# Kernel optimization log

Hardware: AMD Instinct MI355X
Metric: run time of the kernel (lower is better)

The kernel has to match this reference:

```python
import jax, jax.numpy as jnp
import numpy as np

FRONT_FRAC = 0.30   # fraction of lowest-score indices masked (student) / kept (teacher row 0)
RAND_FRAC = 0.10    # fraction of random indices additionally masked for student
# NOTE: the original teacher-mask loop has a reset bug: only row 0 of each batch
# element gets the 'keep only front indices' mask; rows 1..R-1 end up all ones.
# We replicate that behavior faithfully.

def setup_inputs() -> dict:
    key = jax.random.key(0)
    score = jax.random.normal(key, (8, 2048, 4096), dtype=jnp.float32)
    return {"score": score}

def _masks(score):
    B, R, C = score.shape
    k_front = int(C * FRONT_FRAC)
    k_rand = int(C * RAND_FRAC)
    # ascending sort -> indices of the k_front lowest scores per row  [B,R,k_front]
    front = jnp.argsort(score, axis=-1)[..., :k_front]
    # random.sample(range(C), k_rand) per row -> random permutation prefix
    rkey = jax.random.key(42)
    rand_idx = jnp.argsort(jax.random.uniform(rkey, (B, R, C)), axis=-1)[..., :k_rand]
    bb = jnp.arange(B)[:, None, None]
    rr = jnp.arange(R)[None, :, None]
    # student mask: ones, zeroed at front|random indices
    student_mask = jnp.ones((B, R, C), score.dtype)
    student_mask = student_mask.at[bb, rr, front].set(0)
    student_mask = student_mask.at[bb, rr, rand_idx].set(0)
    # teacher mask: row 0 = indicator of front indices; rows 1.. = all ones (original bug)
    teacher_mask = jnp.ones((B, R, C), score.dtype)
    teacher_mask = teacher_mask.at[:, 0, :].set(0)
    bb0 = jnp.arange(B)[:, None]
    teacher_mask = teacher_mask.at[bb0, 0, front[:, 0, :]].set(1)
    return student_mask, teacher_mask

def reference(score):
    B, R, C = score.shape
    student_mask, teacher_mask = _masks(score)
    student = score * student_mask
    teacher = score * teacher_mask
    # original: cat over batch -> [B*R,C], reshape(B,-1,R), transpose(1,2)
    student = student.reshape(B, -1, R).swapaxes(1, 2)
    teacher = teacher.reshape(B, -1, R).swapaxes(1, 2)
    return student, teacher
```

## Files before the change

### kernel.cpp

```cpp
#include <hip/hip_runtime.h>
#include <stdint.h>

#define BB 8
#define RR 2048
#define CC 4096
#define KFRONT 1228
#define KRAND  409
#define NT 256
#define EPT 16
#define ROWS 32
#define PAD 129

__device__ __forceinline__ uint32_t rotl32(uint32_t x, uint32_t r) {
  return (x << r) | (x >> (32u - r));
}

__device__ __forceinline__ uint32_t threefry_bits(uint32_t i) {
  const uint32_t ks0 = 0u, ks1 = 42u;
  const uint32_t ks2 = 0x1BD11BDAu ^ ks0 ^ ks1;
  uint32_t x0 = ks0;
  uint32_t x1 = i + ks1;
#define R4(a, b, c, d)                         \
  x0 += x1; x1 = rotl32(x1, (a)); x1 ^= x0;    \
  x0 += x1; x1 = rotl32(x1, (b)); x1 ^= x0;    \
  x0 += x1; x1 = rotl32(x1, (c)); x1 ^= x0;    \
  x0 += x1; x1 = rotl32(x1, (d)); x1 ^= x0;
  R4(13u, 15u, 26u, 6u)  x0 += ks1; x1 += ks2 + 1u;
  R4(17u, 29u, 16u, 24u) x0 += ks2; x1 += ks0 + 2u;
  R4(13u, 15u, 26u, 6u)  x0 += ks0; x1 += ks1 + 3u;
  R4(17u, 29u, 16u, 24u) x0 += ks1; x1 += ks2 + 4u;
  R4(13u, 15u, 26u, 6u)  x0 += ks2; x1 += ks0 + 5u;
#undef R4
  return x0 ^ x1;
}

struct SelSh {
  uint32_t hist4[4 * 256];
  uint32_t cum[256];
  int sel_digit;
  int sel_below;
};

template <int NPASS>
__device__ uint64_t radix_select(const uint32_t (&keys)[EPT], int tid, int k,
                                 SelSh* sh) {
  uint64_t prefix = 0;
  int kk = k;
  const int wave = tid >> 6;
  for (int p = NPASS - 1; p >= 0; --p) {
    const int shift = 8 * p;
    ((uint4*)sh->hist4)[tid] = make_uint4(0, 0, 0, 0);
    __syncthreads();
#pragma unroll
    for (int j = 0; j < EPT; ++j) {
      uint64_t comp = ((uint64_t)keys[j] << 12) | (uint32_t)(j * NT + tid);
      if ((comp >> (shift + 8)) == prefix)
        atomicAdd(&sh->hist4[wave * 256 + ((uint32_t)(comp >> shift) & 255u)],
                  1u);
    }
    __syncthreads();
    if (tid < 64) {
      uint4 h0 = ((const uint4*)(sh->hist4 + 0))[tid];
      uint4 h1 = ((const uint4*)(sh->hist4 + 256))[tid];
      uint4 h2 = ((const uint4*)(sh->hist4 + 512))[tid];
      uint4 h3 = ((const uint4*)(sh->hist4 + 768))[tid];
      uint32_t s0 = h0.x + h1.x + h2.x + h3.x;
      uint32_t s1 = h0.y + h1.y + h2.y + h3.y;
      uint32_t s2 = h0.z + h1.z + h2.z + h3.z;
      uint32_t s3 = h0.w + h1.w + h2.w + h3.w;
      uint32_t sum = s0 + s1 + s2 + s3;
      uint32_t inc = sum;
      for (int off = 1; off < 64; off <<= 1) {
        uint32_t v = __shfl_up(inc, (unsigned)off);
        if (tid >= off) inc += v;
      }
      uint32_t base = inc - sum;
      ((uint4*)sh->cum)[tid] =
          make_uint4(base + s0, base + s0 + s1, base + s0 + s1 + s2, base + sum);
    }
    __syncthreads();
    int cum = (int)sh->cum[tid];
    int prev = tid ? (int)sh->cum[tid - 1] : 0;
    if (cum >= kk && prev < kk) { sh->sel_digit = tid; sh->sel_below = prev; }
    __syncthreads();
    prefix = (prefix << 8) | (uint32_t)sh->sel_digit;
    kk -= sh->sel_below;
    __syncthreads();
  }
  return prefix;
}

__global__ __launch_bounds__(NT) void fused_kernel(
    const float* __restrict__ score, float* __restrict__ outS,
    float* __restrict__ outT) {
  __shared__ SelSh sh;
  __shared__ uint32_t zbits[ROWS][PAD];
  __shared__ uint32_t fbits[ROWS][PAD];
  __shared__ float tin[ROWS][PAD];

  const int tid = threadIdx.x;
  const int stripe = blockIdx.x;
  const int b = blockIdx.y;
  const int u0 = stripe * 64;
  const int r0 = u0 >> 1;

  for (int rr = 0; rr < ROWS; ++rr) {
    const int rowid = b * RR + (r0 + rr);
    const float* srow = score + (size_t)rowid * CC;
    uint32_t keyS[EPT], keyR[EPT];
#pragma unroll
    for (int j = 0; j < EPT; ++j) {
      int c = j * NT + tid;
      uint32_t fb = __float_as_uint(srow[c]);
      keyS[j] = fb ^ ((uint32_t)((int32_t)fb >> 31) | 0x80000000u);
      keyR[j] = threefry_bits((uint32_t)rowid * (uint32_t)CC + (uint32_t)c) >> 9;
    }
    uint64_t pivF = radix_select<6>(keyS, tid, KFRONT, &sh);
    uint64_t pivR = radix_select<5>(keyR, tid, KRAND, &sh);
#pragma unroll
    for (int j = 0; j < EPT; ++j) {
      int c = j * NT + tid;
      uint64_t compS = ((uint64_t)keyS[j] << 12) | (uint32_t)c;
      uint64_t compR = ((uint64_t)keyR[j] << 12) | (uint32_t)c;
      int isF = (compS <= pivF) ? 1 : 0;
      int isZ = (isF || (compR <= pivR)) ? 1 : 0;
      uint64_t bZ = __ballot(isZ);
      uint64_t bF = __ballot(isF);
      if ((tid & 31) == 0) {
        uint32_t wz = (tid & 32) ? (uint32_t)(bZ >> 32) : (uint32_t)bZ;
        uint32_t wf = (tid & 32) ? (uint32_t)(bF >> 32) : (uint32_t)bF;
        zbits[rr][c >> 5] = wz;
        fbits[rr][c >> 5] = wf;
      }
    }
  }
  __syncthreads();

  const int u_local = tid & 63;
  const int rl = u_local >> 1;
  const int half = u_local & 1;
  const bool isrow0 = (r0 + rl) == 0;
  float* oS = outS + (size_t)b * RR * CC + (size_t)(u0 + u_local);
  float* oT = outT + (size_t)b * RR * CC + (size_t)(u0 + u_local);

  for (int vt = 0; vt < 32; ++vt) {
    const int v0 = vt * 64;
#pragma unroll
    for (int it = 0; it < 16; ++it) {
      int idx = it * NT + tid;
      int lrl = idx >> 7;
      int colsel = (idx >> 6) & 1;
      int lane = idx & 63;
      tin[lrl][colsel * 64 + lane] =
          score[(size_t)(b * RR + r0 + lrl) * CC + colsel * 2048 + v0 + lane];
    }
    __syncthreads();
    const int w0 = half * 64 + (v0 >> 5);
    const uint32_t z0 = zbits[rl][w0], z1 = zbits[rl][w0 + 1];
    const uint32_t f0 = fbits[rl][w0], f1 = fbits[rl][w0 + 1];
#pragma unroll
    for (int it = 0; it < 16; ++it) {
      int vl = it * 4 + (tid >> 6);
      float s = tin[rl][half * 64 + vl];
      uint32_t zw = (vl & 32) ? z1 : z0;
      uint32_t fw = (vl & 32) ? f1 : f0;
      int bit = vl & 31;
      float st = ((zw >> bit) & 1u) ? 0.0f : s;
      float te = isrow0 ? ((((fw >> bit) & 1u)) ? s : 0.0f) : s;
      size_t o = (size_t)(v0 + vl) * CC;
      oS[o] = st;
      oT[o] = te;
    }
    __syncthreads();
  }
}

extern "C" void kernel_launch(void* const* d_in, const int* in_sizes, int n_in,
                              void* d_out, int out_size, void* d_ws,
                              size_t ws_size, hipStream_t stream) {
  const float* score = (const float*)d_in[0];
  float* outS = (float*)d_out;
  float* outT = outS + (size_t)BB * RR * CC;
  dim3 grid(RR / ROWS, BB);
  hipLaunchKernelGGL(fused_kernel, grid, dim3(NT), 0, stream, score, outS,
                     outT);
}
```

Baseline: 1.289 ms.

## Move radix select to per-wavefront rows with early exit and smaller stripes

Each wavefront now owns whole rows (4 rows per wave, 16 rows per block) and runs its radix select with a per-wave LDS histogram and shuffle/ballot scans. This removes the block-wide __syncthreads barriers inside every select pass. The first pass counts 4-bit digits in packed register counters before doing atomics. Passes exit early once the kth element is unique or at an extreme, found by a min/max reduction. Each lane holds 64 keys in registers, which raises register pressure. The output transpose now covers 32 columns per block, so stores are less contiguous per row, and occupancy is hinted at 4 blocks per SM.

Measured after the change: 2.553 ms. 98.1% more time.

```diff
diff --git a/kernel.cpp b/kernel.cpp
--- a/kernel.cpp
+++ b/kernel.cpp
@@ -7,9 +7,8 @@
 #define KFRONT 1228
 #define KRAND  409
 #define NT 256
-#define EPT 16
-#define ROWS 32
-#define PAD 129
+#define ROWS 16
+#define RPW 4
 
 __device__ __forceinline__ uint32_t rotl32(uint32_t x, uint32_t r) {
   return (x << r) | (x >> (32u - r));
@@ -34,140 +33,195 @@
   return x0 ^ x1;
 }
 
-struct SelSh {
-  uint32_t hist4[4 * 256];
-  uint32_t cum[256];
-  int sel_digit;
-  int sel_below;
-};
-
-template <int NPASS>
-__device__ uint64_t radix_select(const uint32_t (&keys)[EPT], int tid, int k,
-                                 SelSh* sh) {
+template <int NPASS, int NB1>
+__device__ __forceinline__ uint64_t wave_select(const uint32_t (&key)[64],
+                                                int lane, int k,
+                                                uint32_t* hist) {
   uint64_t prefix = 0;
+  uint64_t result = 0;
   int kk = k;
-  const int wave = tid >> 6;
-  for (int p = NPASS - 1; p >= 0; --p) {
+
+  auto pick = [&](int shift) -> bool {
+    const uint4 h = *(const uint4*)(hist + 4 * lane);
+    int s0 = (int)h.x, s1 = s0 + (int)h.y, s2 = s1 + (int)h.z,
+        s3 = s2 + (int)h.w;
+    int inc = s3;
+#pragma unroll
+    for (int off = 1; off < 64; off <<= 1) {
+      int v = __shfl_up(inc, (unsigned)off);
+      if (lane >= off) inc += v;
+    }
+    const int base = inc - s3;
+    const uint64_t bal = __ballot(base + s3 >= kk);
+    const int L = __ffsll((unsigned long long)bal) - 1;
+    const int bL = __shfl(base, L);
+    const int a0 = __shfl(s0, L), a1 = __shfl(s1, L), a2 = __shfl(s2, L),
+              a3 = __shfl(s3, L);
+    int dsub, below, cnt;
+    if (kk <= bL + a0)      { dsub = 0; below = bL;      cnt = a0;      }
+    else if (kk <= bL + a1) { dsub = 1; below = bL + a0; cnt = a1 - a0; }
+    else if (kk <= bL + a2) { dsub = 2; below = bL + a1; cnt = a2 - a1; }
+    else                    { dsub = 3; below = bL + a2; cnt = a3 - a2; }
+    prefix = (prefix << 8) | (uint32_t)(4 * L + dsub);
+    kk -= below;
+    if (shift == 0) { result = prefix; return true; }
+    if (cnt == 1 || kk == 1 || kk == cnt) {
+      const bool usemin = (kk == 1 && cnt > 1);
+      uint64_t found = usemin ? ~0ull : 0ull;
+#pragma unroll
+      for (int j = 0; j < 64; ++j) {
+        const uint64_t comp =
+            ((uint64_t)key[j] << 12) | (uint32_t)(j * 64 + lane);
+        if ((comp >> shift) == prefix)
+          found = usemin ? (comp < found ? comp : found)
+                         : (comp > found ? comp : found);
+      }
+#pragma unroll
+      for (int off = 1; off < 64; off <<= 1) {
+        const uint64_t o = (uint64_t)__shfl_xor((unsigned long long)found, off);
+        found = usemin ? (o < found ? o : found) : (o > found ? o : found);
+      }
+      result = found;
+      return true;
+    }
+    return false;
+  };
+
+  {
+    *(uint4*)(hist + 4 * lane) = make_uint4(0, 0, 0, 0);
+    const int ksh = 8 * NPASS - 20;
+    uint64_t c0 = 0, c1 = 0;
+#pragma unroll
+    for (int j = 0; j < 64; ++j) {
+      const uint32_t d = key[j] >> ksh;
+      if constexpr (NB1 <= 8) {
+        c0 += 1ull << (8 * d);
+      } else {
+        if (d < 8) c0 += 1ull << (8 * d);
+        else       c1 += 1ull << (8 * (d - 8));
+      }
+    }
+#pragma unroll
+    for (int b = 0; b < NB1; ++b) {
+      const uint32_t cv =
+          (uint32_t)(((b < 8) ? c0 : c1) >> (8 * (b & 7))) & 0xffu;
+      if (cv) atomicAdd(&hist[b], cv);
+    }
+    if (pick(8 * (NPASS - 1))) return result;
+  }
+#pragma unroll 1
+  for (int p = NPASS - 2; p >= 0; --p) {
     const int shift = 8 * p;
-    ((uint4*)sh->hist4)[tid] = make_uint4(0, 0, 0, 0);
-    __syncthreads();
-#pragma unroll
-    for (int j = 0; j < EPT; ++j) {
-      uint64_t comp = ((uint64_t)keys[j] << 12) | (uint32_t)(j * NT + tid);
+    *(uint4*)(hist + 4 * lane) = make_uint4(0, 0, 0, 0);
+#pragma unroll
+    for (int j = 0; j < 64; ++j) {
+      const uint64_t comp =
+          ((uint64_t)key[j] << 12) | (uint32_t)(j * 64 + lane);
       if ((comp >> (shift + 8)) == prefix)
-        atomicAdd(&sh->hist4[wave * 256 + ((uint32_t)(comp >> shift) & 255u)],
-                  1u);
-    }
-    __syncthreads();
-    if (tid < 64) {
-      uint4 h0 = ((const uint4*)(sh->hist4 + 0))[tid];
-      uint4 h1 = ((const uint4*)(sh->hist4 + 256))[tid];
-      uint4 h2 = ((const uint4*)(sh->hist4 + 512))[tid];
-      uint4 h3 = ((const uint4*)(sh->hist4 + 768))[tid];
-      uint32_t s0 = h0.x + h1.x + h2.x + h3.x;
-      uint32_t s1 = h0.y + h1.y + h2.y + h3.y;
-      uint32_t s2 = h0.z + h1.z + h2.z + h3.z;
-      uint32_t s3 = h0.w + h1.w + h2.w + h3.w;
-      uint32_t sum = s0 + s1 + s2 + s3;
-      uint32_t inc = sum;
-      for (int off = 1; off < 64; off <<= 1) {
-        uint32_t v = __shfl_up(inc, (unsigned)off);
-        if (tid >= off) inc += v;
-      }
-      uint32_t base = inc - sum;
-      ((uint4*)sh->cum)[tid] =
-          make_uint4(base + s0, base + s0 + s1, base + s0 + s1 + s2, base + sum);
-    }
-    __syncthreads();
-    int cum = (int)sh->cum[tid];
-    int prev = tid ? (int)sh->cum[tid - 1] : 0;
-    if (cum >= kk && prev < kk) { sh->sel_digit = tid; sh->sel_below = prev; }
-    __syncthreads();
-    prefix = (prefix << 8) | (uint32_t)sh->sel_digit;
-    kk -= sh->sel_below;
-    __syncthreads();
-  }
-  return prefix;
-}
-
-__global__ __launch_bounds__(NT) void fused_kernel(
+        atomicAdd(&hist[(uint32_t)(comp >> shift) & 255u], 1u);
+    }
+    if (pick(shift)) return result;
+  }
+  return result;
+}
+
+__global__ __launch_bounds__(NT, 4) void fused_kernel(
     const float* __restrict__ score, float* __restrict__ outS,
     float* __restrict__ outT) {
-  __shared__ SelSh sh;
-  __shared__ uint32_t zbits[ROWS][PAD];
-  __shared__ uint32_t fbits[ROWS][PAD];
-  __shared__ float tin[ROWS][PAD];
+  __shared__ __align__(16) uint32_t sh_hist[4 * 256];
+  __shared__ uint32_t zbT[128][17];
+  __shared__ uint32_t fb0[128];
+  __shared__ float tin[ROWS][130];
 
   const int tid = threadIdx.x;
+  const int lane = tid & 63;
+  const int wv = tid >> 6;
   const int stripe = blockIdx.x;
   const int b = blockIdx.y;
-  const int u0 = stripe * 64;
-  const int r0 = u0 >> 1;
-
-  for (int rr = 0; rr < ROWS; ++rr) {
-    const int rowid = b * RR + (r0 + rr);
+  const int r0 = stripe * ROWS;
+  const int u0 = 2 * r0;
+
+  uint32_t* hist = sh_hist + wv * 256;
+
+#pragma unroll 1
+  for (int t = 0; t < RPW; ++t) {
+    const int rl = wv * RPW + t;
+    const int rowid = b * RR + (r0 + rl);
     const float* srow = score + (size_t)rowid * CC;
-    uint32_t keyS[EPT], keyR[EPT];
-#pragma unroll
-    for (int j = 0; j < EPT; ++j) {
-      int c = j * NT + tid;
-      uint32_t fb = __float_as_uint(srow[c]);
-      keyS[j] = fb ^ ((uint32_t)((int32_t)fb >> 31) | 0x80000000u);
-      keyR[j] = threefry_bits((uint32_t)rowid * (uint32_t)CC + (uint32_t)c) >> 9;
-    }
-    uint64_t pivF = radix_select<6>(keyS, tid, KFRONT, &sh);
-    uint64_t pivR = radix_select<5>(keyR, tid, KRAND, &sh);
-#pragma unroll
-    for (int j = 0; j < EPT; ++j) {
-      int c = j * NT + tid;
-      uint64_t compS = ((uint64_t)keyS[j] << 12) | (uint32_t)c;
-      uint64_t compR = ((uint64_t)keyR[j] << 12) | (uint32_t)c;
-      int isF = (compS <= pivF) ? 1 : 0;
-      int isZ = (isF || (compR <= pivR)) ? 1 : 0;
-      uint64_t bZ = __ballot(isZ);
-      uint64_t bF = __ballot(isF);
-      if ((tid & 31) == 0) {
-        uint32_t wz = (tid & 32) ? (uint32_t)(bZ >> 32) : (uint32_t)bZ;
-        uint32_t wf = (tid & 32) ? (uint32_t)(bF >> 32) : (uint32_t)bF;
-        zbits[rr][c >> 5] = wz;
-        fbits[rr][c >> 5] = wf;
-      }
+    uint32_t key[64];
+#pragma unroll
+    for (int j = 0; j < 64; ++j) {
+      const uint32_t fb = __float_as_uint(srow[j * 64 + lane]);
+      key[j] = fb ^ ((uint32_t)((int32_t)fb >> 31) | 0x80000000u);
+    }
+    const uint64_t pivF = wave_select<6, 16>(key, lane, KFRONT, hist);
+    uint64_t fm = 0;
+#pragma unroll
+    for (int j = 0; j < 64; ++j) {
+      const uint64_t comp =
+          ((uint64_t)key[j] << 12) | (uint32_t)(j * 64 + lane);
+      fm |= (uint64_t)(comp <= pivF) << j;
+    }
+    if (r0 + rl == 0) {
+#pragma unroll
+      for (int j = 0; j < 64; ++j) {
+        const uint64_t bf = __ballot((fm >> j) & 1ull);
+        if ((lane & 31) == 0)
+          fb0[2 * j + (lane >> 5)] =
+              (lane & 32) ? (uint32_t)(bf >> 32) : (uint32_t)bf;
+      }
+    }
+#pragma unroll
+    for (int j = 0; j < 64; ++j)
+      key[j] = threefry_bits((uint32_t)rowid * (uint32_t)CC +
+                             (uint32_t)(j * 64 + lane)) >> 9;
+    const uint64_t pivR = wave_select<5, 8>(key, lane, KRAND, hist);
+#pragma unroll
+    for (int j = 0; j < 64; ++j) {
+      const uint64_t comp =
+          ((uint64_t)key[j] << 12) | (uint32_t)(j * 64 + lane);
+      const int isZ = (int)((fm >> j) & 1ull) | (int)(comp <= pivR);
+      const uint64_t bz = __ballot(isZ);
+      if ((lane & 31) == 0)
+        zbT[2 * j + (lane >> 5)][rl] =
+            (lane & 32) ? (uint32_t)(bz >> 32) : (uint32_t)bz;
     }
   }
   __syncthreads();
 
-  const int u_local = tid & 63;
-  const int rl = u_local >> 1;
-  const int half = u_local & 1;
-  const bool isrow0 = (r0 + rl) == 0;
-  float* oS = outS + (size_t)b * RR * CC + (size_t)(u0 + u_local);
-  float* oT = outT + (size_t)b * RR * CC + (size_t)(u0 + u_local);
-
+  const int ul = tid & 31;
+  const int rl2 = ul >> 1;
+  const int half = ul & 1;
+  const bool isrow0 = (r0 + rl2) == 0;
+  float* oS = outS + (size_t)b * RR * CC + (size_t)(u0 + ul);
+  float* oT = outT + (size_t)b * RR * CC + (size_t)(u0 + ul);
+
+#pragma unroll 1
   for (int vt = 0; vt < 32; ++vt) {
     const int v0 = vt * 64;
 #pragma unroll
-    for (int it = 0; it < 16; ++it) {
-      int idx = it * NT + tid;
-      int lrl = idx >> 7;
-      int colsel = (idx >> 6) & 1;
-      int lane = idx & 63;
-      tin[lrl][colsel * 64 + lane] =
-          score[(size_t)(b * RR + r0 + lrl) * CC + colsel * 2048 + v0 + lane];
+    for (int it = 0; it < 8; ++it) {
+      const int idx = it * NT + tid;
+      const int lrl = idx >> 7;
+      const int colsel = (idx >> 6) & 1;
+      const int ll = idx & 63;
+      tin[lrl][colsel * 64 + ll] =
+          score[(size_t)(b * RR + r0 + lrl) * CC + colsel * 2048 + v0 + ll];
     }
     __syncthreads();
     const int w0 = half * 64 + (v0 >> 5);
-    const uint32_t z0 = zbits[rl][w0], z1 = zbits[rl][w0 + 1];
-    const uint32_t f0 = fbits[rl][w0], f1 = fbits[rl][w0 + 1];
-#pragma unroll
-    for (int it = 0; it < 16; ++it) {
-      int vl = it * 4 + (tid >> 6);
-      float s = tin[rl][half * 64 + vl];
-      uint32_t zw = (vl & 32) ? z1 : z0;
-      uint32_t fw = (vl & 32) ? f1 : f0;
-      int bit = vl & 31;
-      float st = ((zw >> bit) & 1u) ? 0.0f : s;
-      float te = isrow0 ? ((((fw >> bit) & 1u)) ? s : 0.0f) : s;
-      size_t o = (size_t)(v0 + vl) * CC;
+    const uint32_t z0 = zbT[w0][rl2], z1 = zbT[w0 + 1][rl2];
+    const uint32_t f0 = fb0[w0], f1 = fb0[w0 + 1];
+#pragma unroll
+    for (int it = 0; it < 8; ++it) {
+      const int vl = it * 8 + (tid >> 5);
+      const float s = tin[rl2][half * 64 + vl];
+      const uint32_t zw = (vl & 32) ? z1 : z0;
+      const uint32_t fw = (vl & 32) ? f1 : f0;
+      const int bit = vl & 31;
+      const float st = ((zw >> bit) & 1u) ? 0.0f : s;
+      const float te = isrow0 ? ((((fw >> bit) & 1u)) ? s : 0.0f) : s;
+      const size_t o = (size_t)(v0 + vl) * CC;
       oS[o] = st;
       oT[o] = te;
     }
```
